# Optimization experiments

Measured on AMD Instinct MI355X. Metric: run time of the kernel, lower is better.

## Reference

```python
import jax, jax.numpy as jnp
import numpy as np

THRESHOLD = 0.045
TAU = 20.0
N = 1048576
H = 128


def setup_inputs() -> dict:
    key = jax.random.key(0)
    ks = jax.random.split(key, 7)
    x = jax.random.normal(ks[0], (N, 1), dtype=jnp.float32)
    s1 = 1.0  # 1/sqrt(fan_in=1)
    s2 = 1.0 / np.sqrt(H).astype(np.float32)
    W1 = jax.random.uniform(ks[1], (H, 1), jnp.float32, -s1, s1)
    b1 = jax.random.uniform(ks[2], (H,), jnp.float32, -s1, s1)
    W2 = jax.random.uniform(ks[3], (H, H), jnp.float32, -s2, s2)
    b2 = jax.random.uniform(ks[4], (H,), jnp.float32, -s2, s2)
    W3 = jax.random.uniform(ks[5], (1, H), jnp.float32, -s2, s2)
    b3 = jax.random.uniform(ks[6], (1,), jnp.float32, -s2, s2)
    return {"x": x, "W1": W1, "b1": b1, "W2": W2, "b2": b2, "W3": W3, "b3": b3}


def reference(x, W1, b1, W2, b2, W3, b3):
    n = x.shape[0]
    # threshold-gated event mask (mask[0] forced active, as in original)
    diff = jnp.abs(x - jnp.roll(x, 1, axis=0))[:, 0]
    mask = (diff > THRESHOLD).at[0].set(True)
    # tiny MLP; computed densely — values at non-active rows are never read
    # (output gathers only last-active rows), so the math matches the
    # original's gather-then-MLP exactly.
    h = jax.nn.relu(x @ W1.T + b1)        # [N, H]
    h = jax.nn.relu(h @ W2.T + b2)        # [N, H]
    y = h @ W3.T + b3                     # [N, 1]
    t = jnp.arange(n, dtype=jnp.float32)
    # last active time <= i  (cumsum(mask)-1 indexing into active rows is
    # equivalent to gathering at the last active position)
    last_t = jax.lax.cummax(jnp.where(mask, t, jnp.float32(0.0)))  # [N]
    last_idx = last_t.astype(jnp.int32)
    decay = jnp.exp(-(t - last_t) / TAU)[:, None]  # [N, 1]
    output = y[last_idx] * decay
    n_active = mask.sum(dtype=jnp.int32)
    return output, n_active
```

## Files before the change

### kernel.cpp

```cpp
#include <hip/hip_runtime.h>
#include <math.h>


#define THRESH   0.045f
#define NH       128
#define TSZ      8192
#define GMIN     -6.0f
#define GMAX     6.0f
#define TPB      256
#define ITEMS    2
#define CHUNK    (TPB * ITEMS)
#define NSCAN    2048
#define NTBLK    256
#define POISON32 0xAAAAAAAAu

__global__ __launch_bounds__(TPB) void kT(const float* __restrict__ W1,
                                          const float* __restrict__ b1,
                                          const float* __restrict__ W2,
                                          const float* __restrict__ b2,
                                          const float* __restrict__ W3,
                                          const float* __restrict__ b3,
                                          float* __restrict__ table) {
  __shared__ float w2s[NH * NH];
  const int t = threadIdx.x, b = blockIdx.x;
  {
    const float4* src = (const float4*)W2;
    float4* dst = (float4*)w2s;
    #pragma unroll
    for (int i = 0; i < (NH * NH / 4) / TPB; ++i)
      dst[t + i * TPB] = src[t + i * TPB];
  }
  __syncthreads();

  const int p  = t & 15;
  const int e0 = b * 32 + (t >> 4) * 2;
  const float step = (GMAX - GMIN) * (1.0f / (float)(TSZ - 1));
  const float xv0 = GMIN + step * (float)e0;
  const float xv1 = xv0 + step;

  float h10[8], h11[8];
  #pragma unroll
  for (int c = 0; c < 2; ++c) {
    #pragma unroll
    for (int r = 0; r < 4; ++r) {
      const int k = 4 * (p + 16 * c) + r;
      const float w = W1[k], bb = b1[k];
      h10[c * 4 + r] = fmaxf(fmaf(xv0, w, bb), 0.0f);
      h11[c * 4 + r] = fmaxf(fmaf(xv1, w, bb), 0.0f);
    }
  }
  const bool hi = (p & 8) != 0;
  float y = 0.0f;
  const float b3v = b3[0];
  #pragma unroll 4
  for (int j = 0; j < NH; ++j) {
    const float* row = &w2s[j * NH];
    float a0 = 0.f, a1 = 0.f, c0 = 0.f, c1 = 0.f;
    #pragma unroll
    for (int c = 0; c < 2; ++c) {
      const float4 w = *(const float4*)&row[4 * (p + 16 * c)];
      a0 = fmaf(h10[c * 4 + 0], w.x, a0);
      a1 = fmaf(h10[c * 4 + 1], w.y, a1);
      a0 = fmaf(h10[c * 4 + 2], w.z, a0);
      a1 = fmaf(h10[c * 4 + 3], w.w, a1);
      c0 = fmaf(h11[c * 4 + 0], w.x, c0);
      c1 = fmaf(h11[c * 4 + 1], w.y, c1);
      c0 = fmaf(h11[c * 4 + 2], w.z, c0);
      c1 = fmaf(h11[c * 4 + 3], w.w, c1);
    }
    const float s0 = a0 + a1, s1 = c0 + c1;
    float u = hi ? s1 : s0;
    float v = hi ? s0 : s1;
    v = __shfl_xor(v, 8);
    u += v;
    u += __shfl_xor(u, 1);
    u += __shfl_xor(u, 2);
    u += __shfl_xor(u, 4);
    const float h2 = fmaxf(u + b2[j], 0.0f);
    y = fmaf(h2, W3[j], y);
  }
  if ((p & 7) == 0) table[e0 + (p >> 3)] = y + b3v;
}

__global__ __launch_bounds__(TPB) void kS(const float* __restrict__ x, int n,
                                          const float* __restrict__ table,
                                          unsigned int* __restrict__ cnts,
                                          float* __restrict__ out) {
  __shared__ int swl[4], swc[4], sred[4];
  __shared__ int sgx;
  const int t = threadIdx.x, b = blockIdx.x;
  const int lane = t & 63, wv = t >> 6;
  const int base = b * CHUNK + t * ITEMS;

  float xs[ITEMS];
  const bool full = (base + ITEMS) <= n;
  if (full) {
    const float2 v = *(const float2*)(x + base);
    xs[0] = v.x; xs[1] = v.y;
  } else {
    #pragma unroll
    for (int it = 0; it < ITEMS; ++it)
      xs[it] = (base + it < n) ? x[base + it] : 0.0f;
  }
  float prev = (base > 0 && base <= n) ? x[base - 1] : 0.0f;
  unsigned m = 0; int tl = -1; int cnt = 0;
  #pragma unroll
  for (int it = 0; it < ITEMS; ++it) {
    const int i = base + it;
    if (i < n) {
      const bool act = (i == 0) || (fabsf(xs[it] - prev) > THRESH);
      if (act) { tl = i; ++cnt; m |= (1u << it); }
      prev = xs[it];
    }
  }

  int incl = tl;
  #pragma unroll
  for (int off = 1; off < 64; off <<= 1) {
    const int v = __shfl_up(incl, off);
    if (lane >= off) incl = max(incl, v);
  }
  int wsum = cnt;
  #pragma unroll
  for (int off = 1; off < 64; off <<= 1) wsum += __shfl_xor(wsum, off);
  if (lane == 63) swl[wv] = incl;
  if (lane == 0)  swc[wv] = wsum;

  if (wv == 0) {
    int g = -1;
    if (b > 0) {
      int ws = b * CHUNK - 64;
      for (;;) {
        const int i = ws + lane;
        const float xi = x[i];
        const float xp = (i > 0) ? x[i - 1] : 0.0f;
        const bool act = (i == 0) || (fabsf(xi - xp) > THRESH);
        const unsigned long long bal = __ballot(act);
        if (bal) { g = ws + 63 - (int)__builtin_clzll(bal); break; }
        ws -= 64;
      }
    }
    if (lane == 0) sgx = g;
  }
  __syncthreads();

  const int exclW = __shfl_up(incl, 1);
  int run = sgx;
  #pragma unroll
  for (int w = 0; w < 4; ++w) if (w < wv) run = max(run, swl[w]);
  if (lane > 0) run = max(run, exclW);

  if (t == 0) {
    const int bcnt = swc[0] + swc[1] + swc[2] + swc[3];
    __hip_atomic_store(&cnts[b], (unsigned)(bcnt + 1),
                       __ATOMIC_RELAXED, __HIP_MEMORY_SCOPE_AGENT);
  }

  const float invstep = (float)(TSZ - 1) / (GMAX - GMIN);
  if (full) {
    float o[ITEMS];
    #pragma unroll
    for (int it = 0; it < ITEMS; ++it) {
      const int i = base + it;
      const bool act = (m >> it) & 1u;
      if (act) run = i;
      const float xj = act ? xs[it] : x[run];
      const float u = (xj - GMIN) * invstep;
      int i0 = (int)u;
      i0 = max(0, min(i0, TSZ - 2));
      const float f = u - (float)i0;
      const float t0 = table[i0], t1 = table[i0 + 1];
      o[it] = fmaf(f, t1 - t0, t0) * __expf((float)(run - i) * 0.05f);
    }
    float2 ov = { o[0], o[1] };
    *(float2*)(out + base) = ov;
  } else {
    #pragma unroll
    for (int it = 0; it < ITEMS; ++it) {
      const int i = base + it;
      if (i >= n) break;
      const bool act = (m >> it) & 1u;
      if (act) run = i;
      const float xj = act ? xs[it] : x[run];
      const float u = (xj - GMIN) * invstep;
      int i0 = (int)u;
      i0 = max(0, min(i0, TSZ - 2));
      const float f = u - (float)i0;
      const float t0 = table[i0], t1 = table[i0 + 1];
      out[i] = fmaf(f, t1 - t0, t0) * __expf((float)(run - i) * 0.05f);
    }
  }

  if (b == 0) {
    int v = 0;
    #pragma unroll
    for (int s8 = 0; s8 < NSCAN / TPB; ++s8) {
      const int idx = t + s8 * TPB;
      unsigned c;
      for (;;) {
        c = __hip_atomic_load(&cnts[idx], __ATOMIC_RELAXED,
                              __HIP_MEMORY_SCOPE_AGENT);
        if (c != POISON32) break;
        __builtin_amdgcn_s_sleep(1);
      }
      v += (int)c - 1;
    }
    #pragma unroll
    for (int off = 1; off < 64; off <<= 1) v += __shfl_xor(v, off);
    if (lane == 0) sred[wv] = v;
    __syncthreads();
    if (t == 0) out[n] = (float)(sred[0] + sred[1] + sred[2] + sred[3]);
  }
}

extern "C" void kernel_launch(void* const* d_in, const int* in_sizes, int n_in,
                              void* d_out, int out_size, void* d_ws, size_t ws_size,
                              hipStream_t stream) {
  const float* x  = (const float*)d_in[0];
  const float* W1 = (const float*)d_in[1];
  const float* b1 = (const float*)d_in[2];
  const float* W2 = (const float*)d_in[3];
  const float* b2 = (const float*)d_in[4];
  const float* W3 = (const float*)d_in[5];
  const float* b3 = (const float*)d_in[6];
  float* out = (float*)d_out;
  const int n = in_sizes[0];

  char* w = (char*)d_ws;
  float* table = (float*)w;
  unsigned int* cnts = (unsigned int*)(w + TSZ * 4);

  kT<<<NTBLK, TPB, 0, stream>>>(W1, b1, W2, b2, W3, b3, table);
  kS<<<NSCAN, TPB, 0, stream>>>(x, n, table, cnts, out);
}
```

Measured before the change: 90.89 us.

## Fuse table-build and scan kernels into one launch with flag sync

Merges the MLP lookup-table build kernel and the scan/interpolation kernel into a single launch. The first 256 blocks build the table and publish per-block release flags, and the scan blocks spin-wait on those flags only right before the table lookup, so their mask and scan work overlaps the table build. The build blocks now read W2 directly from global memory instead of staging it in shared memory. The change removes a kernel launch boundary, but relies on build blocks being scheduled ahead of or alongside the waiting blocks, and it adds atomic loads for the table reads.

```diff
diff --git a/kernel.cpp b/kernel.cpp
--- a/kernel.cpp
+++ b/kernel.cpp
@@ -10,87 +10,86 @@
 #define TPB      256
 #define ITEMS    2
 #define CHUNK    (TPB * ITEMS)
+#define NBUILD   256
 #define NSCAN    2048
-#define NTBLK    256
 #define POISON32 0xAAAAAAAAu
 
-__global__ __launch_bounds__(TPB) void kT(const float* __restrict__ W1,
+__global__ __launch_bounds__(TPB) void kF(const float* __restrict__ x, int n,
+                                          const float* __restrict__ W1,
                                           const float* __restrict__ b1,
                                           const float* __restrict__ W2,
                                           const float* __restrict__ b2,
                                           const float* __restrict__ W3,
                                           const float* __restrict__ b3,
-                                          float* __restrict__ table) {
-  __shared__ float w2s[NH * NH];
+                                          float* __restrict__ table,
+                                          unsigned int* __restrict__ cnts,
+                                          unsigned int* __restrict__ tflag,
+                                          float* __restrict__ out) {
   const int t = threadIdx.x, b = blockIdx.x;
-  {
-    const float4* src = (const float4*)W2;
-    float4* dst = (float4*)w2s;
-    #pragma unroll
-    for (int i = 0; i < (NH * NH / 4) / TPB; ++i)
-      dst[t + i * TPB] = src[t + i * TPB];
-  }
-  __syncthreads();
-
-  const int p  = t & 15;
-  const int e0 = b * 32 + (t >> 4) * 2;
-  const float step = (GMAX - GMIN) * (1.0f / (float)(TSZ - 1));
-  const float xv0 = GMIN + step * (float)e0;
-  const float xv1 = xv0 + step;
-
-  float h10[8], h11[8];
-  #pragma unroll
-  for (int c = 0; c < 2; ++c) {
-    #pragma unroll
-    for (int r = 0; r < 4; ++r) {
-      const int k = 4 * (p + 16 * c) + r;
-      const float w = W1[k], bb = b1[k];
-      h10[c * 4 + r] = fmaxf(fmaf(xv0, w, bb), 0.0f);
-      h11[c * 4 + r] = fmaxf(fmaf(xv1, w, bb), 0.0f);
-    }
-  }
-  const bool hi = (p & 8) != 0;
-  float y = 0.0f;
-  const float b3v = b3[0];
-  #pragma unroll 4
-  for (int j = 0; j < NH; ++j) {
-    const float* row = &w2s[j * NH];
-    float a0 = 0.f, a1 = 0.f, c0 = 0.f, c1 = 0.f;
+  const int lane = t & 63, wv = t >> 6;
+
+  if (b < NBUILD) {
+    const int p  = t & 15;
+    const int e0 = b * 32 + (t >> 4) * 2;
+    const float step = (GMAX - GMIN) * (1.0f / (float)(TSZ - 1));
+    const float xv0 = GMIN + step * (float)e0;
+    const float xv1 = xv0 + step;
+
+    float h10[8], h11[8];
     #pragma unroll
     for (int c = 0; c < 2; ++c) {
-      const float4 w = *(const float4*)&row[4 * (p + 16 * c)];
-      a0 = fmaf(h10[c * 4 + 0], w.x, a0);
-      a1 = fmaf(h10[c * 4 + 1], w.y, a1);
-      a0 = fmaf(h10[c * 4 + 2], w.z, a0);
-      a1 = fmaf(h10[c * 4 + 3], w.w, a1);
-      c0 = fmaf(h11[c * 4 + 0], w.x, c0);
-      c1 = fmaf(h11[c * 4 + 1], w.y, c1);
-      c0 = fmaf(h11[c * 4 + 2], w.z, c0);
-      c1 = fmaf(h11[c * 4 + 3], w.w, c1);
-    }
-    const float s0 = a0 + a1, s1 = c0 + c1;
-    float u = hi ? s1 : s0;
-    float v = hi ? s0 : s1;
-    v = __shfl_xor(v, 8);
-    u += v;
-    u += __shfl_xor(u, 1);
-    u += __shfl_xor(u, 2);
-    u += __shfl_xor(u, 4);
-    const float h2 = fmaxf(u + b2[j], 0.0f);
-    y = fmaf(h2, W3[j], y);
-  }
-  if ((p & 7) == 0) table[e0 + (p >> 3)] = y + b3v;
-}
-
-__global__ __launch_bounds__(TPB) void kS(const float* __restrict__ x, int n,
-                                          const float* __restrict__ table,
-                                          unsigned int* __restrict__ cnts,
-                                          float* __restrict__ out) {
+      #pragma unroll
+      for (int r = 0; r < 4; ++r) {
+        const int k = 4 * (p + 16 * c) + r;
+        const float w = W1[k], bb = b1[k];
+        h10[c * 4 + r] = fmaxf(fmaf(xv0, w, bb), 0.0f);
+        h11[c * 4 + r] = fmaxf(fmaf(xv1, w, bb), 0.0f);
+      }
+    }
+    const bool hi = (p & 8) != 0;
+    float y = 0.0f;
+    const float b3v = b3[0];
+    #pragma unroll 2
+    for (int j = 0; j < NH; ++j) {
+      const float* row = &W2[j * NH];
+      float a0 = 0.f, a1 = 0.f, c0 = 0.f, c1 = 0.f;
+      #pragma unroll
+      for (int c = 0; c < 2; ++c) {
+        const float4 w = *(const float4*)&row[4 * (p + 16 * c)];
+        a0 = fmaf(h10[c * 4 + 0], w.x, a0);
+        a1 = fmaf(h10[c * 4 + 1], w.y, a1);
+        a0 = fmaf(h10[c * 4 + 2], w.z, a0);
+        a1 = fmaf(h10[c * 4 + 3], w.w, a1);
+        c0 = fmaf(h11[c * 4 + 0], w.x, c0);
+        c1 = fmaf(h11[c * 4 + 1], w.y, c1);
+        c0 = fmaf(h11[c * 4 + 2], w.z, c0);
+        c1 = fmaf(h11[c * 4 + 3], w.w, c1);
+      }
+      const float s0 = a0 + a1, s1 = c0 + c1;
+      float u = hi ? s1 : s0;
+      float v = hi ? s0 : s1;
+      v = __shfl_xor(v, 8);
+      u += v;
+      u += __shfl_xor(u, 1);
+      u += __shfl_xor(u, 2);
+      u += __shfl_xor(u, 4);
+      const float h2 = fmaxf(u + b2[j], 0.0f);
+      y = fmaf(h2, W3[j], y);
+    }
+    if ((p & 7) == 0)
+      __hip_atomic_store(&table[e0 + (p >> 3)], y + b3v,
+                         __ATOMIC_RELAXED, __HIP_MEMORY_SCOPE_AGENT);
+    __syncthreads();
+    if (t == 0)
+      __hip_atomic_store(&tflag[b], 1u, __ATOMIC_RELEASE,
+                         __HIP_MEMORY_SCOPE_AGENT);
+    return;
+  }
+
   __shared__ int swl[4], swc[4], sred[4];
   __shared__ int sgx;
-  const int t = threadIdx.x, b = blockIdx.x;
-  const int lane = t & 63, wv = t >> 6;
-  const int base = b * CHUNK + t * ITEMS;
+  const int s = b - NBUILD;
+  const int base = s * CHUNK + t * ITEMS;
 
   float xs[ITEMS];
   const bool full = (base + ITEMS) <= n;
@@ -128,8 +127,8 @@
 
   if (wv == 0) {
     int g = -1;
-    if (b > 0) {
-      int ws = b * CHUNK - 64;
+    if (s > 0) {
+      int ws = s * CHUNK - 64;
       for (;;) {
         const int i = ws + lane;
         const float xi = x[i];
@@ -152,9 +151,19 @@
 
   if (t == 0) {
     const int bcnt = swc[0] + swc[1] + swc[2] + swc[3];
-    __hip_atomic_store(&cnts[b], (unsigned)(bcnt + 1),
+    __hip_atomic_store(&cnts[s], (unsigned)(bcnt + 1),
                        __ATOMIC_RELAXED, __HIP_MEMORY_SCOPE_AGENT);
   }
+
+  {
+    for (;;) {
+      const unsigned f = __hip_atomic_load(&tflag[t], __ATOMIC_RELAXED,
+                                           __HIP_MEMORY_SCOPE_AGENT);
+      if (f == 1u) break;
+      __builtin_amdgcn_s_sleep(2);
+    }
+  }
+  __syncthreads();
 
   const float invstep = (float)(TSZ - 1) / (GMAX - GMIN);
   if (full) {
@@ -169,7 +178,10 @@
       int i0 = (int)u;
       i0 = max(0, min(i0, TSZ - 2));
       const float f = u - (float)i0;
-      const float t0 = table[i0], t1 = table[i0 + 1];
+      const float t0 = __hip_atomic_load(&table[i0], __ATOMIC_RELAXED,
+                                         __HIP_MEMORY_SCOPE_AGENT);
+      const float t1 = __hip_atomic_load(&table[i0 + 1], __ATOMIC_RELAXED,
+                                         __HIP_MEMORY_SCOPE_AGENT);
       o[it] = fmaf(f, t1 - t0, t0) * __expf((float)(run - i) * 0.05f);
     }
     float2 ov = { o[0], o[1] };
@@ -186,12 +198,15 @@
       int i0 = (int)u;
       i0 = max(0, min(i0, TSZ - 2));
       const float f = u - (float)i0;
-      const float t0 = table[i0], t1 = table[i0 + 1];
+      const float t0 = __hip_atomic_load(&table[i0], __ATOMIC_RELAXED,
+                                         __HIP_MEMORY_SCOPE_AGENT);
+      const float t1 = __hip_atomic_load(&table[i0 + 1], __ATOMIC_RELAXED,
+                                         __HIP_MEMORY_SCOPE_AGENT);
       out[i] = fmaf(f, t1 - t0, t0) * __expf((float)(run - i) * 0.05f);
     }
   }
 
-  if (b == 0) {
+  if (s == 0) {
     int v = 0;
     #pragma unroll
     for (int s8 = 0; s8 < NSCAN / TPB; ++s8) {
@@ -201,7 +216,7 @@
         c = __hip_atomic_load(&cnts[idx], __ATOMIC_RELAXED,
                               __HIP_MEMORY_SCOPE_AGENT);
         if (c != POISON32) break;
-        __builtin_amdgcn_s_sleep(1);
+        __builtin_amdgcn_s_sleep(2);
       }
       v += (int)c - 1;
     }
@@ -228,8 +243,9 @@
 
   char* w = (char*)d_ws;
   float* table = (float*)w;
-  unsigned int* cnts = (unsigned int*)(w + TSZ * 4);
-
-  kT<<<NTBLK, TPB, 0, stream>>>(W1, b1, W2, b2, W3, b3, table);
-  kS<<<NSCAN, TPB, 0, stream>>>(x, n, table, cnts, out);
+  unsigned int* cnts  = (unsigned int*)(w + TSZ * 4);
+  unsigned int* tflag = (unsigned int*)(w + TSZ * 4 + NSCAN * 4);
+
+  kF<<<NBUILD + NSCAN, TPB, 0, stream>>>(x, n, W1, b1, W2, b2, W3, b3,
+                                         table, cnts, tflag, out);
 }
```

New measurement: 115.7 us. +27.3%, slower.
